# Performance work log

Hardware: AMD Instinct MI355X
Metric: run time of the kernel (lower is better)

Reference implementation:

```python
import jax, jax.numpy as jnp
import numpy as np

SCALE = 0.08838834764831845  # 1/sqrt(128)

def setup_inputs() -> dict:
    key = jax.random.key(0)
    k1, k2, k3 = jax.random.split(key, 3)
    B, H, Lq, Lk, D = 8, 32, 4, 4096, 128
    q = jax.random.normal(k1, (B, H, Lq, D), dtype=jnp.float32)
    k = jax.random.normal(k2, (B, H, Lk, D), dtype=jnp.float32)
    v = jax.random.normal(k3, (B, H, Lk, D), dtype=jnp.float32)
    attention_mask = jnp.zeros((B, 1, Lq, Lk), dtype=jnp.float32)
    return {"q": q, "k": k, "v": v, "attention_mask": attention_mask}

def reference(q, k, v, attention_mask):
    # scores: [B, H, Lq, Lk]
    scores = jnp.einsum('bhqd,bhkd->bhqk', q, k) * SCALE
    scores = scores + attention_mask  # additive mask, broadcasts over H
    weights = jax.nn.softmax(scores, axis=-1)
    out = jnp.einsum('bhqk,bhkd->bhqd', weights, v)  # [B, H, Lq, D]
    return out
```

## Files before the change

### kernel.cpp

```cpp
#include <hip/hip_runtime.h>
#include <math.h>

#define NB   8
#define NH   32
#define LQ   4
#define LK   4096
#define DD   128
#define SCALE_F 0.08838834764831845f

__global__ __launch_bounds__(1024, 4)
void attn_decode_kernel(const float* __restrict__ Q, const float* __restrict__ K,
                        const float* __restrict__ V, const float* __restrict__ Msk,
                        float* __restrict__ Out)
{
    __shared__ float o_buf[16][LQ][DD];
    __shared__ float ml_buf[16][LQ][2];

    const int bh   = blockIdx.x;
    const int b    = bh >> 5;
    const int tid  = threadIdx.x;
    const int wave = tid >> 6;
    const int lane = tid & 63;
    const int half = lane >> 5;
    const int sub  = lane & 31;

    const float* qp = Q   + (size_t)bh * (LQ * DD);
    const float* kp = K   + (size_t)bh * (LK * DD);
    const float* vp = V   + (size_t)bh * (LK * DD);
    const float* mp = Msk + (size_t)b  * (LQ * LK);

    float4 q4[LQ];
#pragma unroll
    for (int qi = 0; qi < LQ; ++qi)
        q4[qi] = *(const float4*)(qp + qi * DD + sub * 4);

    float m_run[LQ], l_run[LQ];
    float4 o4[LQ];
#pragma unroll
    for (int qi = 0; qi < LQ; ++qi) {
        m_run[qi] = -INFINITY;
        l_run[qi] = 0.0f;
        o4[qi].x = 0.0f; o4[qi].y = 0.0f; o4[qi].z = 0.0f; o4[qi].w = 0.0f;
    }

    for (int s = 0; s < 64; ++s) {
        const int base = s * 64 + wave * 4;
        const int ja = base + half;
        const int jb = ja + 2;

        const float4 ka = *(const float4*)(kp + (size_t)ja * DD + sub * 4);
        const float4 kb = *(const float4*)(kp + (size_t)jb * DD + sub * 4);
        const float4 va = *(const float4*)(vp + (size_t)ja * DD + sub * 4);
        const float4 vb = *(const float4*)(vp + (size_t)jb * DD + sub * 4);

        float sa[LQ], sb[LQ];
#pragma unroll
        for (int qi = 0; qi < LQ; ++qi) {
            sa[qi] = ka.x*q4[qi].x + ka.y*q4[qi].y + ka.z*q4[qi].z + ka.w*q4[qi].w;
            sb[qi] = kb.x*q4[qi].x + kb.y*q4[qi].y + kb.z*q4[qi].z + kb.w*q4[qi].w;
        }
#pragma unroll
        for (int msk = 1; msk <= 16; msk <<= 1) {
#pragma unroll
            for (int qi = 0; qi < LQ; ++qi) {
                sa[qi] += __shfl_xor(sa[qi], msk, 64);
                sb[qi] += __shfl_xor(sb[qi], msk, 64);
            }
        }

#pragma unroll
        for (int qi = 0; qi < LQ; ++qi) {
            const float s_a = sa[qi] * SCALE_F + mp[qi * LK + ja];
            const float s_b = sb[qi] * SCALE_F + mp[qi * LK + jb];
            const float mn  = fmaxf(m_run[qi], fmaxf(s_a, s_b));
            const float f   = __expf(m_run[qi] - mn);
            const float pa  = __expf(s_a - mn);
            const float pb  = __expf(s_b - mn);
            m_run[qi] = mn;
            l_run[qi] = l_run[qi] * f + pa + pb;
            o4[qi].x = o4[qi].x * f + pa * va.x + pb * vb.x;
            o4[qi].y = o4[qi].y * f + pa * va.y + pb * vb.y;
            o4[qi].z = o4[qi].z * f + pa * va.z + pb * vb.z;
            o4[qi].w = o4[qi].w * f + pa * va.w + pb * vb.w;
        }
    }

#pragma unroll
    for (int qi = 0; qi < LQ; ++qi) {
        const float m_o = __shfl_xor(m_run[qi], 32, 64);
        const float l_o = __shfl_xor(l_run[qi], 32, 64);
        float4 oo;
        oo.x = __shfl_xor(o4[qi].x, 32, 64);
        oo.y = __shfl_xor(o4[qi].y, 32, 64);
        oo.z = __shfl_xor(o4[qi].z, 32, 64);
        oo.w = __shfl_xor(o4[qi].w, 32, 64);
        const float M  = fmaxf(m_run[qi], m_o);
        const float fo = __expf(m_run[qi] - M);
        const float fx = __expf(m_o - M);
        o4[qi].x = o4[qi].x * fo + oo.x * fx;
        o4[qi].y = o4[qi].y * fo + oo.y * fx;
        o4[qi].z = o4[qi].z * fo + oo.z * fx;
        o4[qi].w = o4[qi].w * fo + oo.w * fx;
        l_run[qi] = l_run[qi] * fo + l_o * fx;
        m_run[qi] = M;
    }

    if (half == 0) {
#pragma unroll
        for (int qi = 0; qi < LQ; ++qi)
            *(float4*)&o_buf[wave][qi][sub * 4] = o4[qi];
        if (sub == 0) {
#pragma unroll
            for (int qi = 0; qi < LQ; ++qi) {
                ml_buf[wave][qi][0] = m_run[qi];
                ml_buf[wave][qi][1] = l_run[qi];
            }
        }
    }
    __syncthreads();

    if (tid < LQ * DD) {
        const int qi = tid >> 7;
        const int d  = tid & 127;
        float M = -INFINITY;
#pragma unroll
        for (int w = 0; w < 16; ++w)
            M = fmaxf(M, ml_buf[w][qi][0]);
        float Lsum = 0.0f, Osum = 0.0f;
#pragma unroll
        for (int w = 0; w < 16; ++w) {
            const float f = __expf(ml_buf[w][qi][0] - M);
            Lsum += ml_buf[w][qi][1] * f;
            Osum += o_buf[w][qi][d] * f;
        }
        Out[(size_t)bh * (LQ * DD) + tid] = Osum / Lsum;
    }
}

extern "C" void kernel_launch(void* const* d_in, const int* in_sizes, int n_in,
                              void* d_out, int out_size, void* d_ws, size_t ws_size,
                              hipStream_t stream)
{
    const float* q   = (const float*)d_in[0];
    const float* k   = (const float*)d_in[1];
    const float* v   = (const float*)d_in[2];
    const float* msk = (const float*)d_in[3];
    float* out = (float*)d_out;

    attn_decode_kernel<<<dim3(NB * NH), dim3(1024), 0, stream>>>(q, k, v, msk, out);
}
```

Before: 188.7 us.

## Replace online softmax with two-pass exact softmax staged in shared memory

The single-pass online-softmax loop is split into three phases. A QK pass writes all scores to a 64KB shared buffer, a block-wide max/sum reduction turns them into exponentials, and a PV pass accumulates weights times V with no per-step rescaling. This removes the per-step exp and rescale work from the inner loop, but adds extra barriers and splits the K and V streams into separate passes. The larger shared-memory footprint may also reduce occupancy below the launch-bounds target.

```diff
diff --git a/kernel.cpp b/kernel.cpp
--- a/kernel.cpp
+++ b/kernel.cpp
@@ -13,8 +13,10 @@
                         const float* __restrict__ V, const float* __restrict__ Msk,
                         float* __restrict__ Out)
 {
-    __shared__ float o_buf[16][LQ][DD];
-    __shared__ float ml_buf[16][LQ][2];
+    __shared__ float scores[LQ][LK];
+    __shared__ float red_max[LQ][4];
+    __shared__ float red_sum[LQ][4];
+    __shared__ float g_l[LQ];
 
     const int bh   = blockIdx.x;
     const int b    = bh >> 5;
@@ -34,15 +36,6 @@
     for (int qi = 0; qi < LQ; ++qi)
         q4[qi] = *(const float4*)(qp + qi * DD + sub * 4);
 
-    float m_run[LQ], l_run[LQ];
-    float4 o4[LQ];
-#pragma unroll
-    for (int qi = 0; qi < LQ; ++qi) {
-        m_run[qi] = -INFINITY;
-        l_run[qi] = 0.0f;
-        o4[qi].x = 0.0f; o4[qi].y = 0.0f; o4[qi].z = 0.0f; o4[qi].w = 0.0f;
-    }
-
     for (int s = 0; s < 64; ++s) {
         const int base = s * 64 + wave * 4;
         const int ja = base + half;
@@ -50,8 +43,6 @@
 
         const float4 ka = *(const float4*)(kp + (size_t)ja * DD + sub * 4);
         const float4 kb = *(const float4*)(kp + (size_t)jb * DD + sub * 4);
-        const float4 va = *(const float4*)(vp + (size_t)ja * DD + sub * 4);
-        const float4 vb = *(const float4*)(vp + (size_t)jb * DD + sub * 4);
 
         float sa[LQ], sb[LQ];
 #pragma unroll
@@ -67,73 +58,105 @@
                 sb[qi] += __shfl_xor(sb[qi], msk, 64);
             }
         }
+        if (sub == 0) {
+#pragma unroll
+            for (int qi = 0; qi < LQ; ++qi) {
+                scores[qi][ja] = sa[qi] * SCALE_F + mp[qi * LK + ja];
+                scores[qi][jb] = sb[qi] * SCALE_F + mp[qi * LK + jb];
+            }
+        }
+    }
+    __syncthreads();
 
+    {
+        const int g  = tid >> 8;
+        const int r  = tid & 255;
+        const int wg = (tid >> 6) & 3;
+
+        float lm = -INFINITY;
+#pragma unroll
+        for (int k = 0; k < 16; ++k)
+            lm = fmaxf(lm, scores[g][r + k * 256]);
+#pragma unroll
+        for (int msk = 1; msk <= 32; msk <<= 1)
+            lm = fmaxf(lm, __shfl_xor(lm, msk, 64));
+        if (lane == 0) red_max[g][wg] = lm;
+        __syncthreads();
+
+        const float m = fmaxf(fmaxf(red_max[g][0], red_max[g][1]),
+                              fmaxf(red_max[g][2], red_max[g][3]));
+        float ls = 0.0f;
+#pragma unroll
+        for (int k = 0; k < 16; ++k) {
+            const float w = __expf(scores[g][r + k * 256] - m);
+            scores[g][r + k * 256] = w;
+            ls += w;
+        }
+#pragma unroll
+        for (int msk = 1; msk <= 32; msk <<= 1)
+            ls += __shfl_xor(ls, msk, 64);
+        if (lane == 0) red_sum[g][wg] = ls;
+        __syncthreads();
+
+        if (r == 0)
+            g_l[g] = red_sum[g][0] + red_sum[g][1] + red_sum[g][2] + red_sum[g][3];
+    }
+
+    float4 o4[LQ];
+#pragma unroll
+    for (int qi = 0; qi < LQ; ++qi) {
+        o4[qi].x = 0.0f; o4[qi].y = 0.0f; o4[qi].z = 0.0f; o4[qi].w = 0.0f;
+    }
+
+    for (int s = 0; s < 64; ++s) {
+        const int base = s * 64 + wave * 4;
+        const int ja = base + half;
+        const int jb = ja + 2;
+
+        const float4 va = *(const float4*)(vp + (size_t)ja * DD + sub * 4);
+        const float4 vb = *(const float4*)(vp + (size_t)jb * DD + sub * 4);
+
+        float wa[LQ], wb[LQ];
 #pragma unroll
         for (int qi = 0; qi < LQ; ++qi) {
-            const float s_a = sa[qi] * SCALE_F + mp[qi * LK + ja];
-            const float s_b = sb[qi] * SCALE_F + mp[qi * LK + jb];
-            const float mn  = fmaxf(m_run[qi], fmaxf(s_a, s_b));
-            const float f   = __expf(m_run[qi] - mn);
-            const float pa  = __expf(s_a - mn);
-            const float pb  = __expf(s_b - mn);
-            m_run[qi] = mn;
-            l_run[qi] = l_run[qi] * f + pa + pb;
-            o4[qi].x = o4[qi].x * f + pa * va.x + pb * vb.x;
-            o4[qi].y = o4[qi].y * f + pa * va.y + pb * vb.y;
-            o4[qi].z = o4[qi].z * f + pa * va.z + pb * vb.z;
-            o4[qi].w = o4[qi].w * f + pa * va.w + pb * vb.w;
+            wa[qi] = scores[qi][ja];
+            wb[qi] = scores[qi][jb];
+        }
+#pragma unroll
+        for (int qi = 0; qi < LQ; ++qi) {
+            o4[qi].x += wa[qi] * va.x + wb[qi] * vb.x;
+            o4[qi].y += wa[qi] * va.y + wb[qi] * vb.y;
+            o4[qi].z += wa[qi] * va.z + wb[qi] * vb.z;
+            o4[qi].w += wa[qi] * va.w + wb[qi] * vb.w;
         }
     }
 
 #pragma unroll
     for (int qi = 0; qi < LQ; ++qi) {
-        const float m_o = __shfl_xor(m_run[qi], 32, 64);
-        const float l_o = __shfl_xor(l_run[qi], 32, 64);
-        float4 oo;
-        oo.x = __shfl_xor(o4[qi].x, 32, 64);
-        oo.y = __shfl_xor(o4[qi].y, 32, 64);
-        oo.z = __shfl_xor(o4[qi].z, 32, 64);
-        oo.w = __shfl_xor(o4[qi].w, 32, 64);
-        const float M  = fmaxf(m_run[qi], m_o);
-        const float fo = __expf(m_run[qi] - M);
-        const float fx = __expf(m_o - M);
-        o4[qi].x = o4[qi].x * fo + oo.x * fx;
-        o4[qi].y = o4[qi].y * fo + oo.y * fx;
-        o4[qi].z = o4[qi].z * fo + oo.z * fx;
-        o4[qi].w = o4[qi].w * fo + oo.w * fx;
-        l_run[qi] = l_run[qi] * fo + l_o * fx;
-        m_run[qi] = M;
+        o4[qi].x += __shfl_xor(o4[qi].x, 32, 64);
+        o4[qi].y += __shfl_xor(o4[qi].y, 32, 64);
+        o4[qi].z += __shfl_xor(o4[qi].z, 32, 64);
+        o4[qi].w += __shfl_xor(o4[qi].w, 32, 64);
     }
+
+    __syncthreads();
+    float* ob = &scores[0][0];
 
     if (half == 0) {
 #pragma unroll
         for (int qi = 0; qi < LQ; ++qi)
-            *(float4*)&o_buf[wave][qi][sub * 4] = o4[qi];
-        if (sub == 0) {
-#pragma unroll
-            for (int qi = 0; qi < LQ; ++qi) {
-                ml_buf[wave][qi][0] = m_run[qi];
-                ml_buf[wave][qi][1] = l_run[qi];
-            }
-        }
+            *(float4*)&ob[(wave * LQ + qi) * DD + sub * 4] = o4[qi];
     }
     __syncthreads();
 
     if (tid < LQ * DD) {
         const int qi = tid >> 7;
         const int d  = tid & 127;
-        float M = -INFINITY;
+        float Osum = 0.0f;
 #pragma unroll
         for (int w = 0; w < 16; ++w)
-            M = fmaxf(M, ml_buf[w][qi][0]);
-        float Lsum = 0.0f, Osum = 0.0f;
-#pragma unroll
-        for (int w = 0; w < 16; ++w) {
-            const float f = __expf(ml_buf[w][qi][0] - M);
-            Lsum += ml_buf[w][qi][1] * f;
-            Osum += o_buf[w][qi][d] * f;
-        }
-        Out[(size_t)bh * (LQ * DD) + tid] = Osum / Lsum;
+            Osum += ob[(w * LQ + qi) * DD + d];
+        Out[(size_t)bh * (LQ * DD) + tid] = Osum / g_l[qi];
     }
 }
 
```

Measured after the change: 229.3 us. +21.5%, slower.
